# Optimization experiments

Hardware: AMD Instinct MI355X
Metric: run time of the kernel (lower is better)

The kernel has to match this reference:

```python
import jax, jax.numpy as jnp
import numpy as np

TEMPERATURE = 0.5
W_WITHIN = 1.0
W_CROSS = 0.5
MARGIN = 0.1


def setup_inputs() -> dict:
    key = jax.random.key(0)
    k1, k2 = jax.random.split(key)
    features = jax.random.normal(k1, (8192, 256), dtype=jnp.float32)
    gene_labels = jax.random.randint(k2, (8192,), 0, 200, dtype=jnp.int64 if jax.config.jax_enable_x64 else jnp.int32)
    return {"features": features, "gene_labels": gene_labels}


def reference(features, gene_labels):
    B = features.shape[0]
    # L2-normalize rows, full pairwise cosine similarity / temperature
    fn = features / jnp.linalg.norm(features, axis=1, keepdims=True)
    sim = (fn @ fn.T) / TEMPERATURE  # [B, B]

    same = gene_labels[:, None] == gene_labels[None, :]  # [B, B]
    eye = jnp.eye(B, dtype=bool)
    same_off = same & ~eye            # same-gene, off-diagonal (gene_similarity)
    neg = ~same                       # different-gene pairs (cross_gene_mask)
    has_neg = neg.any(axis=1)

    # Per-anchor logsumexp over negatives (sim of anchor i to all different-gene samples)
    neg_sim = jnp.where(neg, sim, -jnp.inf)
    lse_neg = jax.scipy.special.logsumexp(neg_sim, axis=1)
    lse_neg = jnp.where(has_neg, lse_neg, 0.0)  # rows with no negatives are masked out below

    # Within-gene loss: for each unordered same-gene pair (i<j) with gene != -1 and
    # anchor i having >=1 negative: CE([sim_ij, neg_sims_i], label=0)
    #   = -sim_ij + logaddexp(sim_ij, lse_neg_i) = softplus(lse_neg_i - sim_ij)
    upper = jnp.triu(jnp.ones((B, B), dtype=bool), k=1)
    valid_gene = (gene_labels != -1)[:, None]
    pair_mask = same_off & upper & valid_gene & has_neg[:, None]
    within_gene_loss = jnp.where(pair_mask, jax.nn.softplus(lse_neg[:, None] - sim), 0.0).sum()

    # Cross-gene loss: mean over all ordered different-gene pairs of relu(sim - margin)
    cross_cnt = neg.sum()
    cross_sum = jnp.where(neg, jax.nn.relu(sim - MARGIN), 0.0).sum()
    cross_gene_loss = jnp.where(cross_cnt > 0, cross_sum / jnp.maximum(cross_cnt, 1).astype(sim.dtype), 0.0)

    total_loss = W_WITHIN * within_gene_loss + W_CROSS * cross_gene_loss
    num_within_gene_pairs = same_off.sum().astype(sim.dtype)
    num_cross_gene_pairs = cross_cnt
    return total_loss, within_gene_loss, cross_gene_loss, num_within_gene_pairs, num_cross_gene_pairs
```

## Files before the change

kernel.cpp:

```cpp
#include <hip/hip_runtime.h>
#include <math.h>

#define B_N   8192
#define D_K   256
#define NGENE 200
#define MAXN  512

typedef short  bf16x8 __attribute__((ext_vector_type(8)));
typedef float  f32x4  __attribute__((ext_vector_type(4)));

#define OFF_FNBF    0u
#define OFF_LPART   4194304u
#define OFF_HIST    4718592u
#define OFF_OFFS    4719616u
#define OFF_SORTED  4720640u
#define OFF_CROSSP  4753408u
#define OFF_WITHINP 4757504u
#define OFF_CCORR   4758528u

__device__ __forceinline__ unsigned short f2bf(float f) {
    unsigned int u = __float_as_uint(f);
    unsigned int r = u + 0x7fffu + ((u >> 16) & 1u);
    return (unsigned short)(r >> 16);
}
__device__ __forceinline__ float bf2fu(unsigned short h) { return __uint_as_float(((unsigned int)h) << 16); }
__device__ __forceinline__ float bf2f_lo(unsigned int u) { return __uint_as_float(u << 16); }
__device__ __forceinline__ float bf2f_hi(unsigned int u) { return __uint_as_float(u & 0xffff0000u); }

__global__ __launch_bounds__(256) void k_np(const float* __restrict__ feat,
                                            const int* __restrict__ lab,
                                            unsigned short* __restrict__ fnbf,
                                            int* __restrict__ hist,
                                            int* __restrict__ offs,
                                            int* __restrict__ sorted) {
    if (blockIdx.x < 2048) {
        int wave = threadIdx.x >> 6, lane = threadIdx.x & 63;
        int row  = blockIdx.x * 4 + wave;
        const float4* src = reinterpret_cast<const float4*>(feat + (size_t)row * D_K);
        float4 v = src[lane];
        float ss = v.x * v.x + v.y * v.y + v.z * v.z + v.w * v.w;
#pragma unroll
        for (int m = 1; m < 64; m <<= 1) ss += __shfl_xor(ss, m);
        float rn = 1.0f / sqrtf(ss);
        ushort4 o;
        o.x = f2bf(v.x * rn); o.y = f2bf(v.y * rn);
        o.z = f2bf(v.z * rn); o.w = f2bf(v.w * rn);
        reinterpret_cast<ushort4*>(fnbf + (size_t)row * D_K)[lane] = o;
        return;
    }
    __shared__ int sh_hist[256], sh_scan[256], sh_cur[256];
    int t = threadIdx.x;
    sh_hist[t] = 0;
    __syncthreads();
    for (int i = t; i < B_N; i += 256) {
        int lb = lab[i];
        if (lb >= 0 && lb < NGENE) atomicAdd(&sh_hist[lb], 1);
    }
    __syncthreads();
    int v = sh_hist[t];
    sh_scan[t] = v;
    __syncthreads();
#pragma unroll
    for (int d = 1; d < 256; d <<= 1) {
        int x = (t >= d) ? sh_scan[t - d] : 0;
        __syncthreads();
        sh_scan[t] += x;
        __syncthreads();
    }
    int excl = sh_scan[t] - v;
    sh_cur[t] = excl;
    if (t < NGENE) { hist[t] = v; offs[t] = excl; }
    __syncthreads();
    for (int i = t; i < B_N; i += 256) {
        int lb = lab[i];
        if (lb >= 0 && lb < NGENE) {
            int pos = atomicAdd(&sh_cur[lb], 1);
            sorted[pos] = i;
        }
    }
}

#define GLOAD8(arr, vo) do {                                                                   \
    asm volatile("global_load_dwordx4 %0, %1, %2 offset:0"   : "=v"(arr[0]) : "v"(vo), "s"(fb)); \
    asm volatile("global_load_dwordx4 %0, %1, %2 offset:64"  : "=v"(arr[1]) : "v"(vo), "s"(fb)); \
    asm volatile("global_load_dwordx4 %0, %1, %2 offset:128" : "=v"(arr[2]) : "v"(vo), "s"(fb)); \
    asm volatile("global_load_dwordx4 %0, %1, %2 offset:192" : "=v"(arr[3]) : "v"(vo), "s"(fb)); \
    asm volatile("global_load_dwordx4 %0, %1, %2 offset:256" : "=v"(arr[4]) : "v"(vo), "s"(fb)); \
    asm volatile("global_load_dwordx4 %0, %1, %2 offset:320" : "=v"(arr[5]) : "v"(vo), "s"(fb)); \
    asm volatile("global_load_dwordx4 %0, %1, %2 offset:384" : "=v"(arr[6]) : "v"(vo), "s"(fb)); \
    asm volatile("global_load_dwordx4 %0, %1, %2 offset:448" : "=v"(arr[7]) : "v"(vo), "s"(fb)); \
} while (0)

#define GL_LDS16(gp, lp)                                                          \
    __builtin_amdgcn_global_load_lds(                                             \
        (const __attribute__((address_space(1))) unsigned int*)(gp),              \
        (__attribute__((address_space(3))) unsigned int*)(lp), 16, 0, 0)

#define Z4 ((f32x4){0.f, 0.f, 0.f, 0.f})
#define MFMA(A, B, C) __builtin_amdgcn_mfma_f32_16x16x32_bf16(A, B, C, 0, 0, 0)

#define EPI(AC, LS, CS) do {                                    \
    _Pragma("unroll")                                           \
    for (int r = 0; r < 4; ++r) {                               \
        float av = AC[r];                                       \
        LS[r] += __expf(2.0f * av);                             \
        CS += fmaxf(av - 0.05f, 0.f);                           \
    }                                                           \
} while (0)

#define WAIT_VM(n) do { asm volatile("s_waitcnt vmcnt(" #n ")" ::: "memory"); \
                        __builtin_amdgcn_sched_barrier(0); } while (0)

#define STAGE4(BUF, ST) do {                                                       \
    const char* gsb = gw + (unsigned)(ST) * 16384u;                                \
    GL_LDS16(gsb + sv[0], smem_c + (BUF) + sd[0]);                                 \
    GL_LDS16(gsb + sv[1], smem_c + (BUF) + sd[1]);                                 \
    GL_LDS16(gsb + sv[2], smem_c + (BUF) + sd[2]);                                 \
    GL_LDS16(gsb + sv[3], smem_c + (BUF) + sd[3]);                                 \
} while (0)

__global__ __launch_bounds__(256, 2) void k_pairwise(const unsigned short* __restrict__ fnbf,
                                                     unsigned short* __restrict__ l_part,
                                                     float* __restrict__ cross_part) {
    __shared__ __align__(16) char smem_c[32768];
    __shared__ float shc[4];

    int tid = threadIdx.x;
    int wave = tid >> 6, lane = tid & 63;
    int g16 = lane >> 4, l16 = lane & 15;
    int l7 = l16 & 7;

    int b = blockIdx.x;
    int xcd = b & 7, k = b >> 3;
    int cwin = xcd * 4 + (k >> 5);
    int rg   = k & 31;

    int r0 = rg * 256 + wave * 64;
    const unsigned short* fb = fnbf;

    bf16x8 a0[8], a1[8], a2[8], a3[8];
    unsigned voa = (unsigned)(r0 + l16) * 512u + (unsigned)g16 * 16u;
    GLOAD8(a0, voa); voa += 8192u;
    GLOAD8(a1, voa); voa += 8192u;
    GLOAD8(a2, voa); voa += 8192u;
    GLOAD8(a3, voa);

    const char* gw = (const char*)fnbf + (size_t)cwin * 131072u;
    unsigned sv[4], sd[4];
#pragma unroll
    for (int q = 0; q < 4; ++q) {
        int f = wave * 256 + q * 64 + lane;
        int col = f >> 5;
        sv[q] = (unsigned)(col * 512 + (((f & 31) ^ (col & 7)) << 4));
        sd[q] = (unsigned)(f << 4);
    }

    STAGE4(0u, 0);

    float lsum[4][4] = {};
    float cs0 = 0.f, cs1 = 0.f, cs2 = 0.f, cs3 = 0.f;
    int vb = l16 * 512;

#pragma unroll 1
    for (int st = 0; st < 8; ++st) {
        WAIT_VM(0);
        __builtin_amdgcn_s_barrier();
        if (st < 7) STAGE4((unsigned)(((st + 1) & 1) << 14), st + 1);

        const char* base = smem_c + ((st & 1) << 14);
        f32x4 acA0 = Z4, acA1 = Z4, acA2 = Z4, acA3 = Z4;
        f32x4 acB0 = Z4, acB1 = Z4, acB2 = Z4, acB3 = Z4;
#pragma unroll
        for (int ks = 0; ks < 8; ++ks) {
            const char* p = base + (unsigned)(vb + ((((ks << 2) | g16) ^ l7) << 4));
            bf16x8 bv0 = *(const bf16x8*)p;
            bf16x8 bv1 = *(const bf16x8*)(p + 8192);
            acA0 = MFMA(a0[ks], bv0, acA0);
            acA1 = MFMA(a1[ks], bv0, acA1);
            acA2 = MFMA(a2[ks], bv0, acA2);
            acA3 = MFMA(a3[ks], bv0, acA3);
            acB0 = MFMA(a0[ks], bv1, acB0);
            acB1 = MFMA(a1[ks], bv1, acB1);
            acB2 = MFMA(a2[ks], bv1, acB2);
            acB3 = MFMA(a3[ks], bv1, acB3);
        }
        EPI(acA0, lsum[0], cs0); EPI(acA1, lsum[1], cs1);
        EPI(acA2, lsum[2], cs2); EPI(acA3, lsum[3], cs3);
        EPI(acB0, lsum[0], cs0); EPI(acB1, lsum[1], cs1);
        EPI(acB2, lsum[2], cs2); EPI(acB3, lsum[3], cs3);
    }

#pragma unroll
    for (int t = 0; t < 4; ++t)
#pragma unroll
        for (int r = 0; r < 4; ++r) {
            float v = lsum[t][r];
            v += __shfl_xor(v, 1); v += __shfl_xor(v, 2);
            v += __shfl_xor(v, 4); v += __shfl_xor(v, 8);
            if (l16 == 0)
                l_part[(size_t)cwin * B_N + r0 + t * 16 + g16 * 4 + r] = f2bf(v);
        }

    float c = (cs0 + cs1) + (cs2 + cs3);
#pragma unroll
    for (int m = 1; m < 64; m <<= 1) c += __shfl_xor(c, m);
    if (lane == 0) shc[wave] = c;
    __syncthreads();
    if (tid == 0)
        cross_part[cwin * 32 + rg] = shc[0] + shc[1] + shc[2] + shc[3];
}

__device__ __forceinline__ float dot_g(const uint4* __restrict__ fu, int i, int j) {
    const uint4* pa = fu + (size_t)i * 32;
    const uint4* pb = fu + (size_t)j * 32;
    float d = 0.f;
#pragma unroll
    for (int k = 0; k < 32; ++k) {
        uint4 ua = pa[k], ub = pb[k];
        d = fmaf(bf2f_lo(ua.x), bf2f_lo(ub.x), d);
        d = fmaf(bf2f_hi(ua.x), bf2f_hi(ub.x), d);
        d = fmaf(bf2f_lo(ua.y), bf2f_lo(ub.y), d);
        d = fmaf(bf2f_hi(ua.y), bf2f_hi(ub.y), d);
        d = fmaf(bf2f_lo(ua.z), bf2f_lo(ub.z), d);
        d = fmaf(bf2f_hi(ua.z), bf2f_hi(ub.z), d);
        d = fmaf(bf2f_lo(ua.w), bf2f_lo(ub.w), d);
        d = fmaf(bf2f_hi(ua.w), bf2f_hi(ub.w), d);
    }
    return d;
}

__global__ __launch_bounds__(256) void k_within(const unsigned short* __restrict__ fnbf,
                                                const int* __restrict__ hist,
                                                const int* __restrict__ offs,
                                                const int* __restrict__ sorted,
                                                const unsigned short* __restrict__ l_part,
                                                float* __restrict__ within_part,
                                                float* __restrict__ cross_corr) {
    int g = blockIdx.x;
    int n = hist[g], start = offs[g];
    int t = threadIdx.x;
    int wave = t >> 6, lane = t & 63;
    int g16 = lane >> 4, l16 = lane & 15;

    __shared__ float sim[128 * 130];
    __shared__ int   rid[MAXN];
    __shared__ float slse[MAXN];
    __shared__ float red[256];

    for (int idx = t; idx < n; idx += 256) rid[idx] = sorted[start + idx];
    __syncthreads();

    float ccor = 0.f, wsum = 0.f;

    if (n <= 128) {
        int NT = (n + 15) >> 4;
        const bf16x8* fv = reinterpret_cast<const bf16x8*>(fnbf);
        for (int tile = wave; tile < NT * NT; tile += 4) {
            int ti = tile / NT, tj = tile - ti * NT;
            int ia = ti * 16 + l16;
            int ib = tj * 16 + l16;
            int ra = rid[ia < n ? ia : (n - 1)];
            int rb = rid[ib < n ? ib : (n - 1)];
            f32x4 acc = Z4;
#pragma unroll
            for (int ks = 0; ks < 8; ++ks) {
                bf16x8 av = fv[(size_t)ra * 32 + ks * 4 + g16];
                bf16x8 bv = fv[(size_t)rb * 32 + ks * 4 + g16];
                acc = MFMA(av, bv, acc);
            }
            int si = ti * 16 + g16 * 4;
            int sj = tj * 16 + l16;
#pragma unroll
            for (int r = 0; r < 4; ++r)
                sim[(si + r) * 130 + sj] = acc[r];
        }
        __syncthreads();

        for (int i = t; i < n; i += 256) {
            float raw = 0.f;
#pragma unroll
            for (int k = 0; k < 32; ++k) raw += bf2fu(l_part[(size_t)k * B_N + rid[i]]);
            const float* srow = &sim[i * 130];
            float esum = 0.f;
            for (int j = 0; j < n; ++j) {
                float s = 2.0f * srow[j];
                esum += __expf(s);
                ccor += fmaxf(s - 0.1f, 0.f);
            }
            slse[i] = __logf(raw - esum);
        }
        __syncthreads();

        int nn = n * n;
        for (int p = t; p < nn; p += 256) {
            int i = p / n, j = p - i * n;
            if (j <= i) continue;
            float s = 2.0f * sim[i * 130 + j];
            int ai = (rid[i] < rid[j]) ? i : j;
            float x = slse[ai] - s;
            wsum += fmaxf(x, 0.f) + log1pf(__expf(-fabsf(x)));
        }
    } else {
        const uint4* fu = reinterpret_cast<const uint4*>(fnbf);
        for (int i = t; i < n; i += 256) {
            float raw = 0.f;
#pragma unroll
            for (int k = 0; k < 32; ++k) raw += bf2fu(l_part[(size_t)k * B_N + rid[i]]);
            float esum = 0.f;
            for (int j = 0; j < n; ++j) {
                float s = 2.0f * dot_g(fu, rid[i], rid[j]);
                esum += __expf(s);
                ccor += fmaxf(s - 0.1f, 0.f);
            }
            slse[i] = __logf(raw - esum);
        }
        __syncthreads();
        int nn = n * n;
        for (int p = t; p < nn; p += 256) {
            int i = p / n, j = p - i * n;
            if (j <= i) continue;
            float s = 2.0f * dot_g(fu, rid[i], rid[j]);
            int ai = (rid[i] < rid[j]) ? i : j;
            float x = slse[ai] - s;
            wsum += fmaxf(x, 0.f) + log1pf(__expf(-fabsf(x)));
        }
    }

    red[t] = wsum;
    __syncthreads();
#pragma unroll
    for (int d2 = 128; d2 > 0; d2 >>= 1) {
        if (t < d2) red[t] += red[t + d2];
        __syncthreads();
    }
    if (t == 0) within_part[g] = red[0];
    __syncthreads();
    red[t] = ccor;
    __syncthreads();
#pragma unroll
    for (int d2 = 128; d2 > 0; d2 >>= 1) {
        if (t < d2) red[t] += red[t + d2];
        __syncthreads();
    }
    if (t == 0) cross_corr[g] = red[0];
}

__global__ __launch_bounds__(256) void k_finalize(const float* __restrict__ cross_part,
                                                  const float* __restrict__ within_part,
                                                  const float* __restrict__ cross_corr,
                                                  const int* __restrict__ hist,
                                                  float* __restrict__ out) {
    __shared__ float shc[256];
    __shared__ float shw[256];
    __shared__ float shk[256];
    __shared__ long long shs[256];
    int t = threadIdx.x;
    float cs = 0.f;
    for (int i = t; i < 1024; i += 256) cs += cross_part[i];
    float wv = 0.f, cc = 0.f;
    long long s2 = 0;
    if (t < NGENE) {
        wv = within_part[t];
        cc = cross_corr[t];
        long long h = hist[t];
        s2 = h * h;
    }
    shc[t] = cs; shw[t] = wv; shk[t] = cc; shs[t] = s2;
    __syncthreads();
#pragma unroll
    for (int d = 128; d > 0; d >>= 1) {
        if (t < d) {
            shc[t] += shc[t + d]; shw[t] += shw[t + d];
            shk[t] += shk[t + d]; shs[t] += shs[t + d];
        }
        __syncthreads();
    }
    if (t == 0) {
        long long S  = shs[0];
        long long nw = S - (long long)B_N;
        long long nc = (long long)B_N * (long long)B_N - S;
        float cross_total = 2.0f * shc[0] - shk[0];
        float cross_loss = (nc > 0) ? (cross_total / (float)(nc > 1 ? nc : 1)) : 0.f;
        float within     = shw[0];
        out[0] = within + 0.5f * cross_loss;
        out[1] = within;
        out[2] = cross_loss;
        out[3] = (float)nw;
        out[4] = (float)nc;
    }
}

extern "C" void kernel_launch(void* const* d_in, const int* in_sizes, int n_in,
                              void* d_out, int out_size, void* d_ws, size_t ws_size,
                              hipStream_t stream) {
    const float* feat = (const float*)d_in[0];
    const int*   lab  = (const int*)d_in[1];
    float* out = (float*)d_out;
    char* ws = (char*)d_ws;

    unsigned short* fnbf   = (unsigned short*)(ws + OFF_FNBF);
    unsigned short* l_part = (unsigned short*)(ws + OFF_LPART);
    int*   hist            = (int*)(ws + OFF_HIST);
    int*   offs            = (int*)(ws + OFF_OFFS);
    int*   sorted          = (int*)(ws + OFF_SORTED);
    float* cross_part      = (float*)(ws + OFF_CROSSP);
    float* within_part     = (float*)(ws + OFF_WITHINP);
    float* cross_corr      = (float*)(ws + OFF_CCORR);

    k_np<<<2049, 256, 0, stream>>>(feat, lab, fnbf, hist, offs, sorted);
    k_pairwise<<<1024, 256, 0, stream>>>(fnbf, l_part, cross_part);
    k_within<<<NGENE, 256, 0, stream>>>(fnbf, hist, offs, sorted, l_part, within_part, cross_corr);
    k_finalize<<<1, 256, 0, stream>>>(cross_part, within_part, cross_corr, hist, out);
}
```

Measured before the change: 102.8 us.

## Exploit similarity symmetry to compute only upper-triangular tile pairs

```diff
diff --git a/kernel.cpp b/kernel.cpp
--- a/kernel.cpp
+++ b/kernel.cpp
@@ -99,11 +99,12 @@
 #define Z4 ((f32x4){0.f, 0.f, 0.f, 0.f})
 #define MFMA(A, B, C) __builtin_amdgcn_mfma_f32_16x16x32_bf16(A, B, C, 0, 0, 0)
 
-#define EPI(AC, LS, CS) do {                                    \
+#define EPI2(AC, LS, CE, CS) do {                               \
     _Pragma("unroll")                                           \
     for (int r = 0; r < 4; ++r) {                               \
         float av = AC[r];                                       \
-        LS[r] += __expf(2.0f * av);                             \
+        float e = __expf(2.0f * av);                            \
+        LS[r] += e; CE += e;                                    \
         CS += fmaxf(av - 0.05f, 0.f);                           \
     }                                                           \
 } while (0)
@@ -123,6 +124,7 @@
                                                      unsigned short* __restrict__ l_part,
                                                      float* __restrict__ cross_part) {
     __shared__ __align__(16) char smem_c[32768];
+    __shared__ float colsumws[1024];
     __shared__ float shc[4];
 
     int tid = threadIdx.x;
@@ -130,13 +132,16 @@
     int g16 = lane >> 4, l16 = lane & 15;
     int l7 = l16 & 7;
 
-    int b = blockIdx.x;
-    int xcd = b & 7, k = b >> 3;
-    int cwin = xcd * 4 + (k >> 5);
-    int rg   = k & 31;
+    int b = blockIdx.x, rg = 0, rem = b;
+    while (rem >= 32 - rg) { rem -= 32 - rg; ++rg; }
+    int cw = rg + rem;
+    bool offd = (rg != cw);
 
     int r0 = rg * 256 + wave * 64;
     const unsigned short* fb = fnbf;
+
+#pragma unroll
+    for (int k2 = 0; k2 < 4; ++k2) colsumws[wave * 256 + lane * 4 + k2] = 0.f;
 
     bf16x8 a0[8], a1[8], a2[8], a3[8];
     unsigned voa = (unsigned)(r0 + l16) * 512u + (unsigned)g16 * 16u;
@@ -145,7 +150,7 @@
     GLOAD8(a2, voa); voa += 8192u;
     GLOAD8(a3, voa);
 
-    const char* gw = (const char*)fnbf + (size_t)cwin * 131072u;
+    const char* gw = (const char*)fnbf + (size_t)cw * 131072u;
     unsigned sv[4], sd[4];
 #pragma unroll
     for (int q = 0; q < 4; ++q) {
@@ -184,10 +189,20 @@
             acB2 = MFMA(a2[ks], bv1, acB2);
             acB3 = MFMA(a3[ks], bv1, acB3);
         }
-        EPI(acA0, lsum[0], cs0); EPI(acA1, lsum[1], cs1);
-        EPI(acA2, lsum[2], cs2); EPI(acA3, lsum[3], cs3);
-        EPI(acB0, lsum[0], cs0); EPI(acB1, lsum[1], cs1);
-        EPI(acB2, lsum[2], cs2); EPI(acB3, lsum[3], cs3);
+        float ceA = 0.f, ceB = 0.f;
+        EPI2(acA0, lsum[0], ceA, cs0); EPI2(acA1, lsum[1], ceA, cs1);
+        EPI2(acA2, lsum[2], ceA, cs2); EPI2(acA3, lsum[3], ceA, cs3);
+        EPI2(acB0, lsum[0], ceB, cs0); EPI2(acB1, lsum[1], ceB, cs1);
+        EPI2(acB2, lsum[2], ceB, cs2); EPI2(acB3, lsum[3], ceB, cs3);
+
+        if (offd) {
+            ceA += __shfl_xor(ceA, 16); ceA += __shfl_xor(ceA, 32);
+            ceB += __shfl_xor(ceB, 16); ceB += __shfl_xor(ceB, 32);
+            if (g16 == 0) {
+                colsumws[wave * 256 + st * 32 + l16]      += ceA;
+                colsumws[wave * 256 + st * 32 + 16 + l16] += ceB;
+            }
+        }
     }
 
 #pragma unroll
@@ -198,16 +213,25 @@
             v += __shfl_xor(v, 1); v += __shfl_xor(v, 2);
             v += __shfl_xor(v, 4); v += __shfl_xor(v, 8);
             if (l16 == 0)
-                l_part[(size_t)cwin * B_N + r0 + t * 16 + g16 * 4 + r] = f2bf(v);
-        }
+                l_part[(size_t)cw * B_N + r0 + t * 16 + g16 * 4 + r] = f2bf(v);
+        }
+
+    __syncthreads();
+
+    if (offd) {
+        float cs = colsumws[tid] + colsumws[256 + tid] + colsumws[512 + tid] + colsumws[768 + tid];
+        l_part[(size_t)rg * B_N + cw * 256 + tid] = f2bf(cs);
+    }
 
     float c = (cs0 + cs1) + (cs2 + cs3);
 #pragma unroll
     for (int m = 1; m < 64; m <<= 1) c += __shfl_xor(c, m);
     if (lane == 0) shc[wave] = c;
     __syncthreads();
-    if (tid == 0)
-        cross_part[cwin * 32 + rg] = shc[0] + shc[1] + shc[2] + shc[3];
+    if (tid == 0) {
+        float tot = shc[0] + shc[1] + shc[2] + shc[3];
+        cross_part[b] = offd ? 2.0f * tot : tot;
+    }
 }
 
 __device__ __forceinline__ float dot_g(const uint4* __restrict__ fu, int i, int j) {
@@ -356,7 +380,7 @@
     __shared__ long long shs[256];
     int t = threadIdx.x;
     float cs = 0.f;
-    for (int i = t; i < 1024; i += 256) cs += cross_part[i];
+    for (int i = t; i < 528; i += 256) cs += cross_part[i];
     float wv = 0.f, cc = 0.f;
     long long s2 = 0;
     if (t < NGENE) {
@@ -408,7 +432,7 @@
     float* cross_corr      = (float*)(ws + OFF_CCORR);
 
     k_np<<<2049, 256, 0, stream>>>(feat, lab, fnbf, hist, offs, sorted);
-    k_pairwise<<<1024, 256, 0, stream>>>(fnbf, l_part, cross_part);
+    k_pairwise<<<528, 256, 0, stream>>>(fnbf, l_part, cross_part);
     k_within<<<NGENE, 256, 0, stream>>>(fnbf, hist, offs, sorted, l_part, within_part, cross_corr);
     k_finalize<<<1, 256, 0, stream>>>(cross_part, within_part, cross_corr, hist, out);
 }
```

After: 105.9 us. 1.03x slower.
